# Kernel tuning notes

Hardware: AMD Instinct MI355X
Metric: run time of the kernel (lower is better)

Reference implementation:

```python
import jax, jax.numpy as jnp
import numpy as np

N_NODES = 50000
N_EDGES = 400000
F_IN = 70
E_DIM = 4
HID = 128
HEADS = 4


def _add_self_loops(src, dst, edge_attr, n):
    # PyG GATConv(add_self_loops=True, fill_value='mean' when edge_dim is set):
    # self-loop edge_attr = per-dst-node mean of incoming edge_attr.
    cnt = jax.ops.segment_sum(jnp.ones((src.shape[0],), edge_attr.dtype), dst, n)
    loop_attr = jax.ops.segment_sum(edge_attr, dst, n) / jnp.clip(cnt, 1.0)[:, None]
    loop = jnp.arange(n, dtype=src.dtype)
    return (jnp.concatenate([src, loop]), jnp.concatenate([dst, loop]),
            jnp.concatenate([edge_attr, loop_attr], axis=0))


def _gat_layer(x, src, dst, e_attr, W, a_src, a_dst, We, a_edge, b, concat):
    # W: [in, H*D]; a_src/a_dst/a_edge: [H, D]; We: [edge_dim, H*D]
    n = x.shape[0]
    H, D = a_src.shape
    xs = (x @ W).reshape(n, H, D)                      # [N,H,D]
    s_src = jnp.einsum('nhd,hd->nh', xs, a_src)        # [N,H]
    s_dst = jnp.einsum('nhd,hd->nh', xs, a_dst)
    ee = (e_attr @ We).reshape(-1, H, D)               # [E,H,D]
    s_edge = jnp.einsum('ehd,hd->eh', ee, a_edge)
    alpha = jax.nn.leaky_relu(s_src[src] + s_dst[dst] + s_edge, 0.2)  # [E,H]
    # segment softmax over edges grouped by destination node
    m = jax.ops.segment_max(alpha, dst, n)
    m = jnp.where(jnp.isfinite(m), m, 0.0)
    ex = jnp.exp(alpha - m[dst])
    denom = jax.ops.segment_sum(ex, dst, n)
    alpha = ex / (denom[dst] + 1e-16)
    msg = xs[src] * alpha[..., None]                   # [E,H,D] -- dominant traffic
    agg = jax.ops.segment_sum(msg, dst, n)             # [N,H,D]
    out = agg.reshape(n, H * D) if concat else agg.mean(axis=1)
    return out + b


def _layer_norm(x, g, b, eps=1e-5):
    mu = x.mean(-1, keepdims=True)
    var = ((x - mu) ** 2).mean(-1, keepdims=True)
    return (x - mu) * jax.lax.rsqrt(var + eps) * g + b


def setup_inputs() -> dict:
    key = jax.random.key(0)
    ks = jax.random.split(key, 24)
    f32 = jnp.float32
    node_features = jax.random.normal(ks[0], (N_NODES, F_IN), f32)
    edge_index = jax.random.randint(ks[1], (2, N_EDGES), 0, N_NODES, jnp.int32)
    edge_attr = jax.random.uniform(ks[2], (N_EDGES, E_DIM), f32)
    s = 0.1
    return {
        'node_features': node_features,
        'edge_index': edge_index,
        'edge_attr': edge_attr,
        'W1': jax.random.normal(ks[3], (F_IN, HEADS * HID), f32) * s,
        'as1': jax.random.normal(ks[4], (HEADS, HID), f32) * s,
        'ad1': jax.random.normal(ks[5], (HEADS, HID), f32) * s,
        'We1': jax.random.normal(ks[6], (E_DIM, HEADS * HID), f32) * s,
        'ae1': jax.random.normal(ks[7], (HEADS, HID), f32) * s,
        'b1': jnp.zeros((HEADS * HID,), f32),
        # GAT layer 2: 512 -> 128, 1 head, mean
        'W2': jax.random.normal(ks[8], (HEADS * HID, HID), f32) * s,
        'as2': jax.random.normal(ks[9], (1, HID), f32) * s,
        'ad2': jax.random.normal(ks[10], (1, HID), f32) * s,
        'We2': jax.random.normal(ks[11], (E_DIM, HID), f32) * s,
        'ae2': jax.random.normal(ks[12], (1, HID), f32) * s,
        'b2': jnp.zeros((HID,), f32),
        'ln_g': jnp.ones((HID,), f32),
        'ln_b': jnp.zeros((HID,), f32),
        'pw': jax.random.normal(ks[13], (HID, 8), f32) * s,
        'pb': jnp.zeros((8,), f32),
        'dw': jax.random.normal(ks[14], (HID, 4), f32) * s,
        'db': jnp.zeros((4,), f32),
    }


def reference(node_features, edge_index, edge_attr, W1, as1, ad1, We1, ae1, b1,
              W2, as2, ad2, We2, ae2, b2, ln_g, ln_b, pw, pb, dw, db):
    n = node_features.shape[0]
    src, dst, ea = _add_self_loops(edge_index[0], edge_index[1], edge_attr, n)
    x = jax.nn.gelu(_gat_layer(node_features, src, dst, ea, W1, as1, ad1, We1, ae1, b1, True), approximate=False)
    x = jax.nn.gelu(_gat_layer(x, src, dst, ea, W2, as2, ad2, We2, ae2, b2, False), approximate=False)
    x = _layer_norm(x, ln_g, ln_b)
    return (x @ pw + pb, x @ dw + db)
```

## Files before the change

### kernel.cpp

```cpp
#include <hip/hip_runtime.h>
#include <hip/hip_bf16.h>
#include <math.h>

#define NN 50000
#define NE 400000
#define FIN 70
#define EDIM 4
#define HIDD 128
#define NHEAD 4
constexpr int ET = NE + NN;
constexpr int KP1 = 96;
constexpr int NFP = 72;
constexpr int SCB = (NN + 255) / 256;

constexpr size_t al4(size_t x){ return (x + 3) & ~size_t(3); }
constexpr size_t CNT_O   = 0;
constexpr size_t ZEND    = al4(CNT_O + NN);
constexpr size_t CSR_O   = ZEND;
constexpr size_t BSUM_O  = al4(CSR_O + NN + 1);
constexpr size_t BOFF_O  = al4(BSUM_O + 256);
constexpr size_t EPK_O   = al4(BOFF_O + 256);
constexpr size_t EXF1_O  = al4(EPK_O + (size_t)ET*4);
constexpr size_t EXF2_O  = al4(EXF1_O + (size_t)ET*4);
constexpr size_t SS1_O   = al4(EXF2_O + ET);
constexpr size_t SD1_O   = al4(SS1_O + (size_t)NN*4);
constexpr size_t SS2_O   = al4(SD1_O + (size_t)NN*4);
constexpr size_t SD2_O   = al4(SS2_O + NN);
constexpr size_t CST_O   = al4(SD2_O + NN);
constexpr size_t W1T_O   = al4(CST_O + 2048);
constexpr size_t W2T_O   = al4(W1T_O + 4*128*KP1/2);
constexpr size_t NFB_O   = al4(W2T_O + 128*512/2);
constexpr size_t AGG_O   = al4(NFB_O + (size_t)NN*NFP/2);
constexpr size_t XS2_O   = al4(AGG_O + (size_t)4*NN*KP1/2);

constexpr int VS1 = 0;
constexpr int VD1 = 320;
constexpr int VE1 = 640;
constexpr int VE2 = 656;
constexpr int VS2 = 704;
constexpr int VD2 = 1216;

typedef short s8v __attribute__((ext_vector_type(8)));
typedef float f4v __attribute__((ext_vector_type(4)));

__device__ __forceinline__ unsigned short f2b(float v){
  __hip_bfloat16 b = __float2bfloat16(v);
  return *(unsigned short*)&b;
}
__device__ __forceinline__ float b2f(unsigned u_lo16){
  return __uint_as_float(u_lo16 << 16);
}
__device__ __forceinline__ unsigned pk2(float lo, float hi){
  return (unsigned)f2b(lo) | ((unsigned)f2b(hi) << 16);
}
__device__ __forceinline__ float lrelu(float x){ return x > 0.f ? x : 0.2f * x; }

__device__ __forceinline__ float gelu_fast(float x){
  float z = x * 0.70710678118654752440f;
  float a = fabsf(z);
  float t = 1.f / (1.f + 0.3275911f * a);
  float p = ((((1.061405429f*t - 1.453152027f)*t + 1.421413741f)*t
              - 0.284496736f)*t + 0.254829592f)*t;
  float erfv = 1.f - p * __expf(-a * a);
  erfv = copysignf(erfv, z);
  return 0.5f * x * (1.f + erfv);
}

__global__ void k_deg(const int* __restrict__ ei, int* __restrict__ cnt){
  int e = blockIdx.x * 256 + threadIdx.x;
  if (e >= NE) return;
  atomicAdd(&cnt[ei[NE + e]], 1);
}

__global__ void k_scan1(const int* __restrict__ cnt, int* __restrict__ bsum){
  __shared__ int ws[4];
  int t = threadIdx.x, lane = t & 63, w = t >> 6;
  int i = blockIdx.x * 256 + t;
  int v = (i < NN) ? cnt[i] + 1 : 0;
  for (int o = 32; o; o >>= 1) v += __shfl_down(v, o);
  if (lane == 0) ws[w] = v;
  __syncthreads();
  if (t == 0) bsum[blockIdx.x] = ws[0] + ws[1] + ws[2] + ws[3];
}

__global__ void k_scan2(const int* __restrict__ bsum, int* __restrict__ boff){
  __shared__ int ws[4];
  int t = threadIdx.x, lane = t & 63, w = t >> 6;
  int v = (t < SCB) ? bsum[t] : 0;
  int x = v;
  #pragma unroll
  for (int o = 1; o < 64; o <<= 1){ int u = __shfl_up(x, o); if (lane >= o) x += u; }
  if (lane == 63) ws[w] = x;
  __syncthreads();
  if (w == 0 && lane < 4){
    int y = ws[lane];
    #pragma unroll
    for (int o = 1; o < 4; o <<= 1){ int u = __shfl_up(y, o); if (lane >= o) y += u; }
    ws[lane] = y;
  }
  __syncthreads();
  int incl = x + (w > 0 ? ws[w - 1] : 0);
  if (t < SCB) boff[t] = incl - v;
}

__global__ void k_scan3(const int* __restrict__ cnt, const int* __restrict__ boff,
                        int* __restrict__ csr){
  __shared__ int ws[4];
  int t = threadIdx.x, lane = t & 63, w = t >> 6;
  int i = blockIdx.x * 256 + t;
  int v = (i < NN) ? cnt[i] + 1 : 0;
  int x = v;
  #pragma unroll
  for (int o = 1; o < 64; o <<= 1){ int u = __shfl_up(x, o); if (lane >= o) x += u; }
  if (lane == 63) ws[w] = x;
  __syncthreads();
  if (w == 0 && lane < 4){
    int y = ws[lane];
    #pragma unroll
    for (int o = 1; o < 4; o <<= 1){ int u = __shfl_up(y, o); if (lane >= o) y += u; }
    ws[lane] = y;
  }
  __syncthreads();
  if (i < NN) csr[i + 1] = boff[blockIdx.x] + (w > 0 ? ws[w - 1] : 0) + x;
  if (i == 0) csr[0] = 0;
}

__global__ void k_fill(const int* __restrict__ ei, const float* __restrict__ ea,
                       const int* __restrict__ csr, int* __restrict__ cnt,
                       int4* __restrict__ epk, const float* __restrict__ ss1,
                       const float* __restrict__ sd1, const float* __restrict__ C,
                       float4* __restrict__ exf){
  int e = blockIdx.x * 256 + threadIdx.x;
  if (e >= NE) return;
  int s = ei[e], d = ei[NE + e];
  int r = atomicSub(&cnt[d], 1);
  int p = csr[d] + r - 1;
  float4 a = *(const float4*)&ea[(size_t)e * 4];
  epk[p] = make_int4(s, d, (int)pk2(a.x, a.y), (int)pk2(a.z, a.w));
  float4 ssv = *(const float4*)&ss1[(size_t)s * 4];
  float4 sdv = *(const float4*)&sd1[(size_t)d * 4];
  float e0 = __expf(lrelu(ssv.x + sdv.x + a.x*C[VE1+0] + a.y*C[VE1+4] + a.z*C[VE1+8]  + a.w*C[VE1+12]));
  float e1 = __expf(lrelu(ssv.y + sdv.y + a.x*C[VE1+1] + a.y*C[VE1+5] + a.z*C[VE1+9]  + a.w*C[VE1+13]));
  float e2 = __expf(lrelu(ssv.z + sdv.z + a.x*C[VE1+2] + a.y*C[VE1+6] + a.z*C[VE1+10] + a.w*C[VE1+14]));
  float e3 = __expf(lrelu(ssv.w + sdv.w + a.x*C[VE1+3] + a.y*C[VE1+7] + a.z*C[VE1+11] + a.w*C[VE1+15]));
  exf[p] = make_float4(e0, e1, e2, e3);
}

__global__ void k_loopself(const int* __restrict__ csr, int4* __restrict__ epk,
                           const float* __restrict__ ss1, const float* __restrict__ sd1,
                           const float* __restrict__ C, float4* __restrict__ exf){
  int n = blockIdx.x * 256 + threadIdx.x;
  if (n >= NN) return;
  int a = csr[n], b = csr[n + 1];
  int deg = b - a - 1;
  float s0 = 0.f, s1 = 0.f, s2 = 0.f, s3 = 0.f;
  for (int p = a; p < b - 1; ++p){
    int4 v = epk[p];
    s0 += b2f((unsigned)v.z & 0xffffu); s1 += b2f((unsigned)v.z >> 16);
    s2 += b2f((unsigned)v.w & 0xffffu); s3 += b2f((unsigned)v.w >> 16);
  }
  float inv = 1.f / (float)(deg > 1 ? deg : 1);
  float m0 = s0*inv, m1 = s1*inv, m2 = s2*inv, m3 = s3*inv;
  epk[b - 1] = make_int4(n, n, (int)pk2(m0, m1), (int)pk2(m2, m3));
  float4 ssv = *(const float4*)&ss1[(size_t)n * 4];
  float4 sdv = *(const float4*)&sd1[(size_t)n * 4];
  float e0 = __expf(lrelu(ssv.x + sdv.x + m0*C[VE1+0] + m1*C[VE1+4] + m2*C[VE1+8]  + m3*C[VE1+12]));
  float e1 = __expf(lrelu(ssv.y + sdv.y + m0*C[VE1+1] + m1*C[VE1+5] + m2*C[VE1+9]  + m3*C[VE1+13]));
  float e2 = __expf(lrelu(ssv.z + sdv.z + m0*C[VE1+2] + m1*C[VE1+6] + m2*C[VE1+10] + m3*C[VE1+14]));
  float e3 = __expf(lrelu(ssv.w + sdv.w + m0*C[VE1+3] + m1*C[VE1+7] + m2*C[VE1+11] + m3*C[VE1+15]));
  exf[b - 1] = make_float4(e0, e1, e2, e3);
}

__global__ void k_prep(const float* __restrict__ W1, const float* __restrict__ as1,
                       const float* __restrict__ ad1, const float* __restrict__ We1,
                       const float* __restrict__ ae1, const float* __restrict__ W2,
                       const float* __restrict__ as2, const float* __restrict__ ad2,
                       const float* __restrict__ We2, const float* __restrict__ ae2,
                       float* __restrict__ C){
  int t = threadIdx.x;
  if (t < 280){
    int k = t >> 2, h = t & 3;
    float s = 0.f, d = 0.f;
    for (int dd = 0; dd < 128; ++dd){
      float w = W1[k*512 + h*128 + dd];
      s += w * as1[h*128 + dd];
      d += w * ad1[h*128 + dd];
    }
    C[VS1 + t] = s; C[VD1 + t] = d;
  }
  if (t < 16){
    int k = t >> 2, h = t & 3;
    float s = 0.f;
    for (int dd = 0; dd < 128; ++dd) s += We1[k*512 + h*128 + dd] * ae1[h*128 + dd];
    C[VE1 + t] = s;
  }
  if (t < 4){
    float s = 0.f;
    for (int dd = 0; dd < 128; ++dd) s += We2[t*128 + dd] * ae2[dd];
    C[VE2 + t] = s;
  }
  {
    float s = 0.f, d = 0.f;
    for (int dd = 0; dd < 128; ++dd){
      float w = W2[t*128 + dd];
      s += w * as2[dd];
      d += w * ad2[dd];
    }
    C[VS2 + t] = s; C[VD2 + t] = d;
  }
}

__global__ void k_tw(const float* __restrict__ W1, const float* __restrict__ W2,
                     unsigned short* __restrict__ W1t, unsigned short* __restrict__ W2t){
  int i = blockIdx.x * 256 + threadIdx.x;
  if (i < 4*128*KP1){
    int k = i % KP1, n = (i / KP1) & 127, h = i / (KP1*128);
    float v = (k < FIN) ? W1[k*512 + h*128 + n] : 0.f;
    W1t[i] = f2b(v);
  } else {
    int j = i - 4*128*KP1;
    if (j < 128*512){
      int k = j & 511, n = j >> 9;
      W2t[j] = f2b(W2[k*128 + n]);
    }
  }
}

__global__ __launch_bounds__(256) void k_cnfs1(const float* __restrict__ nf,
    const float* __restrict__ C, unsigned short* __restrict__ nfb,
    float* __restrict__ ss1, float* __restrict__ sd1){
  int lane = threadIdx.x & 63, w = threadIdx.x >> 6;
  int n = blockIdx.x * 4 + w;
  if (n >= NN) return;
  int c0 = lane * 2;
  bool act = lane < 35;
  float v0 = 0.f, v1 = 0.f;
  if (act){
    v0 = nf[(size_t)n * FIN + c0];
    v1 = nf[(size_t)n * FIN + c0 + 1];
  }
  if (lane < 36) *(unsigned*)&nfb[(size_t)n * NFP + c0] = act ? pk2(v0, v1) : 0u;
  float sh[4] = {0,0,0,0}, dh[4] = {0,0,0,0};
  if (act){
    float4 cs0 = *(const float4*)&C[VS1 + c0*4];
    float4 cs1 = *(const float4*)&C[VS1 + (c0+1)*4];
    float4 cd0 = *(const float4*)&C[VD1 + c0*4];
    float4 cd1 = *(const float4*)&C[VD1 + (c0+1)*4];
    sh[0] = v0*cs0.x + v1*cs1.x; sh[1] = v0*cs0.y + v1*cs1.y;
    sh[2] = v0*cs0.z + v1*cs1.z; sh[3] = v0*cs0.w + v1*cs1.w;
    dh[0] = v0*cd0.x + v1*cd1.x; dh[1] = v0*cd0.y + v1*cd1.y;
    dh[2] = v0*cd0.z + v1*cd1.z; dh[3] = v0*cd0.w + v1*cd1.w;
  }
  #pragma unroll
  for (int o = 32; o; o >>= 1){
    #pragma unroll
    for (int h = 0; h < 4; ++h){
      sh[h] += __shfl_xor(sh[h], o);
      dh[h] += __shfl_xor(dh[h], o);
    }
  }
  if (lane == 0){
    *(float4*)&ss1[(size_t)n*4] = make_float4(sh[0], sh[1], sh[2], sh[3]);
    *(float4*)&sd1[(size_t)n*4] = make_float4(dh[0], dh[1], dh[2], dh[3]);
  }
}

__global__ void k_al2(const int4* __restrict__ epk, const float* __restrict__ ss2,
                      const float* __restrict__ sd2, const float* __restrict__ C,
                      float* __restrict__ ex2){
  int p = blockIdx.x * 256 + threadIdx.x;
  if (p >= ET) return;
  int4 pk = epk[p];
  int s = pk.x, d = pk.y;
  float ax = b2f((unsigned)pk.z & 0xffffu), ay = b2f((unsigned)pk.z >> 16);
  float az = b2f((unsigned)pk.w & 0xffffu), aw = b2f((unsigned)pk.w >> 16);
  ex2[p] = __expf(lrelu(ss2[s] + sd2[d] +
             ax*C[VE2] + ay*C[VE2+1] + az*C[VE2+2] + aw*C[VE2+3]));
}

__global__ __launch_bounds__(256) void k_gemm12(
    const unsigned short* __restrict__ agg, const unsigned short* __restrict__ W1t,
    const unsigned short* __restrict__ W2t, const float* __restrict__ b1,
    const float* __restrict__ Cv, unsigned short* __restrict__ xs2b,
    float* __restrict__ ss2, float* __restrict__ sd2){
  __shared__ unsigned short xt[32 * 520];
  __shared__ unsigned short Bs[128 * 40];
  __shared__ unsigned short As[32 * 40];
  int tid = threadIdx.x, lane = tid & 63, w = tid >> 6;
  int wm = w & 1, wn = w >> 1;
  int m15 = lane & 15, rq = lane >> 4;
  int r0 = blockIdx.x * 32;
  constexpr size_t HS = (size_t)NN * KP1;
  for (int h = 0; h < 4; ++h){
    f4v acc[4] = {};
    const unsigned short* Ah = agg + (size_t)h * HS;
    const unsigned short* Wh = W1t + h * 128 * KP1;
    for (int k0 = 0; k0 < KP1; k0 += 32){
      if (tid < 128){
        int r = tid >> 2, c = tid & 3;
        int gr = r0 + r; if (gr >= NN) gr = NN - 1;
        *(uint4*)&As[r*40 + c*8] = *(const uint4*)&Ah[(size_t)gr*KP1 + k0 + c*8];
      }
      #pragma unroll
      for (int i = 0; i < 2; ++i){
        int idx = tid + i*256;
        int r = idx >> 2, c = idx & 3;
        *(uint4*)&Bs[r*40 + c*8] = *(const uint4*)&Wh[r*KP1 + k0 + c*8];
      }
      __syncthreads();
      s8v af = *(const s8v*)&As[(wm*16 + m15)*40 + rq*8];
      #pragma unroll
      for (int ni = 0; ni < 4; ++ni){
        s8v bf = *(const s8v*)&Bs[(wn*64 + ni*16 + m15)*40 + rq*8];
        acc[ni] = __builtin_amdgcn_mfma_f32_16x16x32_bf16(bf, af, acc[ni], 0, 0, 0);
      }
      __syncthreads();
    }
    int lr = wm*16 + m15;
    #pragma unroll
    for (int ni = 0; ni < 4; ++ni){
      int cb = h*128 + wn*64 + ni*16 + rq*4;
      float4 bv = *(const float4*)&b1[cb];
      float v0 = gelu_fast(acc[ni][0] + bv.x);
      float v1 = gelu_fast(acc[ni][1] + bv.y);
      float v2 = gelu_fast(acc[ni][2] + bv.z);
      float v3 = gelu_fast(acc[ni][3] + bv.w);
      *(uint2*)&xt[lr*520 + cb] = make_uint2(pk2(v0,v1), pk2(v2,v3));
    }
  }
  f4v acc2[4] = {};
  for (int k0 = 0; k0 < 512; k0 += 32){
    #pragma unroll
    for (int i = 0; i < 2; ++i){
      int idx = tid + i*256;
      int r = idx >> 2, c = idx & 3;
      *(uint4*)&Bs[r*40 + c*8] = *(const uint4*)&W2t[r*512 + k0 + c*8];
    }
    __syncthreads();
    s8v af = *(const s8v*)&xt[(wm*16 + m15)*520 + k0 + rq*8];
    #pragma unroll
    for (int ni = 0; ni < 4; ++ni){
      s8v bf = *(const s8v*)&Bs[(wn*64 + ni*16 + m15)*40 + rq*8];
      acc2[ni] = __builtin_amdgcn_mfma_f32_16x16x32_bf16(bf, af, acc2[ni], 0, 0, 0);
    }
    __syncthreads();
  }
  int grow = r0 + wm*16 + m15;
  if (grow < NN){
    #pragma unroll
    for (int ni = 0; ni < 4; ++ni){
      int gc = wn*64 + ni*16 + rq*4;
      *(uint2*)&xs2b[(size_t)grow*128 + gc] =
          make_uint2(pk2(acc2[ni][0], acc2[ni][1]), pk2(acc2[ni][2], acc2[ni][3]));
    }
  }
  int row = tid >> 3, ch = tid & 7;
  float sa = 0.f, sdv = 0.f;
  #pragma unroll
  for (int jj = 0; jj < 8; ++jj){
    int j2 = (jj + ch) & 7;
    int cb = ch*64 + j2*8;
    s8v xv = *(const s8v*)&xt[row*520 + cb];
    #pragma unroll
    for (int t2 = 0; t2 < 8; ++t2){
      float xf = b2f((unsigned short)xv[t2]);
      sa  += xf * Cv[VS2 + cb + t2];
      sdv += xf * Cv[VD2 + cb + t2];
    }
  }
  #pragma unroll
  for (int o = 1; o < 8; o <<= 1){ sa += __shfl_xor(sa, o); sdv += __shfl_xor(sdv, o); }
  if (ch == 0 && r0 + row < NN){ ss2[r0 + row] = sa; sd2[r0 + row] = sdv; }
}

__global__ __launch_bounds__(256) void k_aggnf(const int* __restrict__ csr,
    const int4* __restrict__ epk, const float4* __restrict__ exf,
    const unsigned short* __restrict__ nfb, unsigned short* __restrict__ agg){
  int lane = threadIdx.x & 63, w = threadIdx.x >> 6;
  int n = blockIdx.x * 4 + w;
  if (n >= NN) return;
  int off = __builtin_amdgcn_readfirstlane(csr[n]);
  int end = __builtin_amdgcn_readfirstlane(csr[n + 1]);
  int col = lane * 2;
  bool act = lane < 36;
  float d0=0,d1=0,d2=0,d3=0;
  float a00=0,a01=0,a10=0,a11=0,a20=0,a21=0,a30=0,a31=0;
  int p = off;
  for (; p + 2 <= end; p += 2){
    int s0 = epk[p].x, s1 = epk[p+1].x;
    float4 e0 = exf[p], e1 = exf[p+1];
    unsigned u0 = 0, u1 = 0;
    if (act){
      u0 = *(const unsigned*)&nfb[(size_t)s0 * NFP + col];
      u1 = *(const unsigned*)&nfb[(size_t)s1 * NFP + col];
    }
    d0 += e0.x + e1.x; d1 += e0.y + e1.y; d2 += e0.z + e1.z; d3 += e0.w + e1.w;
    float v00 = b2f(u0 & 0xffffu), v01 = b2f(u0 >> 16);
    float v10 = b2f(u1 & 0xffffu), v11 = b2f(u1 >> 16);
    a00 += e0.x*v00 + e1.x*v10; a01 += e0.x*v01 + e1.x*v11;
    a10 += e0.y*v00 + e1.y*v10; a11 += e0.y*v01 + e1.y*v11;
    a20 += e0.z*v00 + e1.z*v10; a21 += e0.z*v01 + e1.z*v11;
    a30 += e0.w*v00 + e1.w*v10; a31 += e0.w*v01 + e1.w*v11;
  }
  if (p < end){
    int s0 = epk[p].x;
    float4 e0 = exf[p];
    unsigned u0 = 0;
    if (act) u0 = *(const unsigned*)&nfb[(size_t)s0 * NFP + col];
    d0 += e0.x; d1 += e0.y; d2 += e0.z; d3 += e0.w;
    float v00 = b2f(u0 & 0xffffu), v01 = b2f(u0 >> 16);
    a00 += e0.x*v00; a01 += e0.x*v01;
    a10 += e0.y*v00; a11 += e0.y*v01;
    a20 += e0.z*v00; a21 += e0.z*v01;
    a30 += e0.w*v00; a31 += e0.w*v01;
  }
  float i0 = 1.f/(d0+1e-16f), i1 = 1.f/(d1+1e-16f);
  float i2 = 1.f/(d2+1e-16f), i3 = 1.f/(d3+1e-16f);
  constexpr size_t HS = (size_t)NN * KP1;
  size_t base = (size_t)n * KP1 + col;
  if (act){
    *(unsigned*)&agg[base]        = pk2(a00*i0, a01*i0);
    *(unsigned*)&agg[base +   HS] = pk2(a10*i1, a11*i1);
    *(unsigned*)&agg[base + 2*HS] = pk2(a20*i2, a21*i2);
    *(unsigned*)&agg[base + 3*HS] = pk2(a30*i3, a31*i3);
  } else if (lane < 48){
    *(unsigned*)&agg[base]        = 0u;
    *(unsigned*)&agg[base +   HS] = 0u;
    *(unsigned*)&agg[base + 2*HS] = 0u;
    *(unsigned*)&agg[base + 3*HS] = 0u;
  }
}

__global__ __launch_bounds__(256) void k_agg2(
    const int* __restrict__ csr, const int4* __restrict__ epk,
    const float* __restrict__ ex2, const unsigned short* __restrict__ xs2b,
    const float* __restrict__ b2, const float* __restrict__ lng,
    const float* __restrict__ lnb, const float* __restrict__ pw,
    const float* __restrict__ pb, const float* __restrict__ dwm,
    const float* __restrict__ dbv, float* __restrict__ out){
  int lane = threadIdx.x & 63, w = threadIdx.x >> 6;
  int n = blockIdx.x * 4 + w;
  if (n >= NN) return;
  int off = __builtin_amdgcn_readfirstlane(csr[n]);
  int end = __builtin_amdgcn_readfirstlane(csr[n + 1]);
  int c0 = lane * 2;
  float acc0 = 0.f, acc1 = 0.f, den = 0.f;
  int p = off;
  for (; p + 4 <= end; p += 4){
    int s0 = epk[p].x, s1 = epk[p+1].x, s2 = epk[p+2].x, s3 = epk[p+3].x;
    float e0 = ex2[p], e1 = ex2[p+1], e2 = ex2[p+2], e3 = ex2[p+3];
    unsigned u0 = *(const unsigned*)&xs2b[(size_t)s0 * 128 + c0];
    unsigned u1 = *(const unsigned*)&xs2b[(size_t)s1 * 128 + c0];
    unsigned u2 = *(const unsigned*)&xs2b[(size_t)s2 * 128 + c0];
    unsigned u3 = *(const unsigned*)&xs2b[(size_t)s3 * 128 + c0];
    den += (e0 + e1) + (e2 + e3);
    acc0 += e0*b2f(u0 & 0xffffu) + e1*b2f(u1 & 0xffffu)
          + e2*b2f(u2 & 0xffffu) + e3*b2f(u3 & 0xffffu);
    acc1 += e0*b2f(u0 >> 16) + e1*b2f(u1 >> 16)
          + e2*b2f(u2 >> 16) + e3*b2f(u3 >> 16);
  }
  for (; p + 2 <= end; p += 2){
    int s0 = epk[p].x, s1 = epk[p+1].x;
    float e0 = ex2[p], e1 = ex2[p+1];
    unsigned u0 = *(const unsigned*)&xs2b[(size_t)s0 * 128 + c0];
    unsigned u1 = *(const unsigned*)&xs2b[(size_t)s1 * 128 + c0];
    den += e0 + e1;
    acc0 += e0*b2f(u0 & 0xffffu) + e1*b2f(u1 & 0xffffu);
    acc1 += e0*b2f(u0 >> 16) + e1*b2f(u1 >> 16);
  }
  if (p < end){
    int s0 = epk[p].x;
    float e0 = ex2[p];
    unsigned u0 = *(const unsigned*)&xs2b[(size_t)s0 * 128 + c0];
    den += e0;
    acc0 += e0*b2f(u0 & 0xffffu);
    acc1 += e0*b2f(u0 >> 16);
  }
  float invd = 1.f / (den + 1e-16f);
  float g0 = gelu_fast(acc0 * invd + b2[c0]);
  float g1 = gelu_fast(acc1 * invd + b2[c0 + 1]);
  float s = g0 + g1;
  #pragma unroll
  for (int o = 32; o; o >>= 1) s += __shfl_xor(s, o);
  float mu = s * (1.f / 128.f);
  float e0 = g0 - mu, e1 = g1 - mu;
  float q = e0*e0 + e1*e1;
  #pragma unroll
  for (int o = 32; o; o >>= 1) q += __shfl_xor(q, o);
  float rstd = rsqrtf(q * (1.f / 128.f) + 1e-5f);
  float y0 = e0 * rstd * lng[c0] + lnb[c0];
  float y1 = e1 * rstd * lng[c0 + 1] + lnb[c0 + 1];
  float pr[12];
  #pragma unroll
  for (int jj = 0; jj < 8; ++jj) pr[jj] = y0 * pw[c0*8 + jj] + y1 * pw[(c0+1)*8 + jj];
  #pragma unroll
  for (int jj = 0; jj < 4; ++jj) pr[8+jj] = y0 * dwm[c0*4 + jj] + y1 * dwm[(c0+1)*4 + jj];
  #pragma unroll
  for (int o = 32; o; o >>= 1)
    #pragma unroll
    for (int jj = 0; jj < 12; ++jj) pr[jj] += __shfl_xor(pr[jj], o);
  if (lane == 0){
    #pragma unroll
    for (int jj = 0; jj < 8; ++jj) out[(size_t)n*8 + jj] = pr[jj] + pb[jj];
    #pragma unroll
    for (int jj = 0; jj < 4; ++jj) out[(size_t)NN*8 + (size_t)n*4 + jj] = pr[8+jj] + dbv[jj];
  }
}

extern "C" void kernel_launch(void* const* d_in, const int* in_sizes, int n_in,
                              void* d_out, int out_size, void* d_ws, size_t ws_size,
                              hipStream_t stream){
  const float* nf  = (const float*)d_in[0];
  const int*   ei  = (const int*)  d_in[1];
  const float* ea  = (const float*)d_in[2];
  const float* W1  = (const float*)d_in[3];
  const float* as1 = (const float*)d_in[4];
  const float* ad1 = (const float*)d_in[5];
  const float* We1 = (const float*)d_in[6];
  const float* ae1 = (const float*)d_in[7];
  const float* b1  = (const float*)d_in[8];
  const float* W2  = (const float*)d_in[9];
  const float* as2 = (const float*)d_in[10];
  const float* ad2 = (const float*)d_in[11];
  const float* We2 = (const float*)d_in[12];
  const float* ae2 = (const float*)d_in[13];
  const float* b2  = (const float*)d_in[14];
  const float* lng = (const float*)d_in[15];
  const float* lnb = (const float*)d_in[16];
  const float* pw  = (const float*)d_in[17];
  const float* pb  = (const float*)d_in[18];
  const float* dw  = (const float*)d_in[19];
  const float* db  = (const float*)d_in[20];
  float* out = (float*)d_out;

  float* wf = (float*)d_ws;
  int*      cnt  = (int*)     (wf + CNT_O);
  int*      csr  = (int*)     (wf + CSR_O);
  int*      bsum = (int*)     (wf + BSUM_O);
  int*      boff = (int*)     (wf + BOFF_O);
  int4*     epk  = (int4*)    (wf + EPK_O);
  float4*   exf1 = (float4*)  (wf + EXF1_O);
  float*    ex2  =            (wf + EXF2_O);
  float*    ss1  =            (wf + SS1_O);
  float*    sd1  =            (wf + SD1_O);
  float*    ss2  =            (wf + SS2_O);
  float*    sd2  =            (wf + SD2_O);
  float*    Cc   =            (wf + CST_O);
  unsigned short* W1t = (unsigned short*)(wf + W1T_O);
  unsigned short* W2t = (unsigned short*)(wf + W2T_O);
  unsigned short* nfb = (unsigned short*)(wf + NFB_O);
  unsigned short* agg = (unsigned short*)(wf + AGG_O);
  unsigned short* xs2b= (unsigned short*)(wf + XS2_O);

  hipMemsetAsync(cnt, 0, NN * sizeof(int), stream);
  k_prep<<<1, 512, 0, stream>>>(W1, as1, ad1, We1, ae1, W2, as2, ad2, We2, ae2, Cc);
  k_tw<<<(4*128*KP1 + 128*512 + 255) / 256, 256, 0, stream>>>(W1, W2, W1t, W2t);
  k_cnfs1<<<(NN + 3) / 4, 256, 0, stream>>>(nf, Cc, nfb, ss1, sd1);
  k_deg<<<(NE + 255) / 256, 256, 0, stream>>>(ei, cnt);
  k_scan1<<<SCB, 256, 0, stream>>>(cnt, bsum);
  k_scan2<<<1, 256, 0, stream>>>(bsum, boff);
  k_scan3<<<SCB, 256, 0, stream>>>(cnt, boff, csr);
  k_fill<<<(NE + 255) / 256, 256, 0, stream>>>(ei, ea, csr, cnt, epk, ss1, sd1, Cc, exf1);
  k_loopself<<<(NN + 255) / 256, 256, 0, stream>>>(csr, epk, ss1, sd1, Cc, exf1);
  k_aggnf<<<(NN + 3) / 4, 256, 0, stream>>>(csr, epk, exf1, nfb, agg);
  k_gemm12<<<(NN + 31) / 32, 256, 0, stream>>>(agg, W1t, W2t, b1, Cc, xs2b, ss2, sd2);
  k_al2<<<(ET + 255) / 256, 256, 0, stream>>>(epk, ss2, sd2, Cc, ex2);
  k_agg2<<<(NN + 3) / 4, 256, 0, stream>>>(csr, epk, ex2, xs2b,
                                           b2, lng, lnb, pw, pb, dw, db, out);
}
```

Baseline: 372.4 us.

## Load GEMM fragments directly from global memory and fuse attention score dot products

```diff
diff --git a/kernel.cpp b/kernel.cpp
--- a/kernel.cpp
+++ b/kernel.cpp
@@ -284,39 +284,31 @@
     const float* __restrict__ Cv, unsigned short* __restrict__ xs2b,
     float* __restrict__ ss2, float* __restrict__ sd2){
   __shared__ unsigned short xt[32 * 520];
-  __shared__ unsigned short Bs[128 * 40];
-  __shared__ unsigned short As[32 * 40];
+  __shared__ float ssp[32][2], sdp[32][2];
   int tid = threadIdx.x, lane = tid & 63, w = tid >> 6;
   int wm = w & 1, wn = w >> 1;
   int m15 = lane & 15, rq = lane >> 4;
   int r0 = blockIdx.x * 32;
+  int lrow = wm * 16 + m15;
+  int grow = r0 + lrow;
+  int growc = grow < NN ? grow : NN - 1;
   constexpr size_t HS = (size_t)NN * KP1;
+  float s2a = 0.f, s2d = 0.f;
+  #pragma unroll
   for (int h = 0; h < 4; ++h){
+    const unsigned short* Ah = agg + (size_t)h * HS + (size_t)growc * KP1;
+    const unsigned short* Wh = W1t + h * 128 * KP1;
     f4v acc[4] = {};
-    const unsigned short* Ah = agg + (size_t)h * HS;
-    const unsigned short* Wh = W1t + h * 128 * KP1;
-    for (int k0 = 0; k0 < KP1; k0 += 32){
-      if (tid < 128){
-        int r = tid >> 2, c = tid & 3;
-        int gr = r0 + r; if (gr >= NN) gr = NN - 1;
-        *(uint4*)&As[r*40 + c*8] = *(const uint4*)&Ah[(size_t)gr*KP1 + k0 + c*8];
-      }
-      #pragma unroll
-      for (int i = 0; i < 2; ++i){
-        int idx = tid + i*256;
-        int r = idx >> 2, c = idx & 3;
-        *(uint4*)&Bs[r*40 + c*8] = *(const uint4*)&Wh[r*KP1 + k0 + c*8];
-      }
-      __syncthreads();
-      s8v af = *(const s8v*)&As[(wm*16 + m15)*40 + rq*8];
+    #pragma unroll
+    for (int kk = 0; kk < 3; ++kk){
+      int k0 = kk * 32;
+      s8v af = *(const s8v*)&Ah[k0 + rq*8];
       #pragma unroll
       for (int ni = 0; ni < 4; ++ni){
-        s8v bf = *(const s8v*)&Bs[(wn*64 + ni*16 + m15)*40 + rq*8];
+        s8v bf = *(const s8v*)&Wh[(wn*64 + ni*16 + m15)*KP1 + k0 + rq*8];
         acc[ni] = __builtin_amdgcn_mfma_f32_16x16x32_bf16(bf, af, acc[ni], 0, 0, 0);
       }
-      __syncthreads();
-    }
-    int lr = wm*16 + m15;
+    }
     #pragma unroll
     for (int ni = 0; ni < 4; ++ni){
       int cb = h*128 + wn*64 + ni*16 + rq*4;
@@ -325,27 +317,31 @@
       float v1 = gelu_fast(acc[ni][1] + bv.y);
       float v2 = gelu_fast(acc[ni][2] + bv.z);
       float v3 = gelu_fast(acc[ni][3] + bv.w);
-      *(uint2*)&xt[lr*520 + cb] = make_uint2(pk2(v0,v1), pk2(v2,v3));
-    }
+      float4 cs = *(const float4*)&Cv[VS2 + cb];
+      float4 cd = *(const float4*)&Cv[VD2 + cb];
+      s2a += v0*cs.x + v1*cs.y + v2*cs.z + v3*cs.w;
+      s2d += v0*cd.x + v1*cd.y + v2*cd.z + v3*cd.w;
+      *(uint2*)&xt[lrow*520 + cb] = make_uint2(pk2(v0,v1), pk2(v2,v3));
+    }
+  }
+  s2a += __shfl_xor(s2a, 16); s2a += __shfl_xor(s2a, 32);
+  s2d += __shfl_xor(s2d, 16); s2d += __shfl_xor(s2d, 32);
+  if (rq == 0){ ssp[lrow][wn] = s2a; sdp[lrow][wn] = s2d; }
+  __syncthreads();
+  if (tid < 32 && r0 + tid < NN){
+    ss2[r0 + tid] = ssp[tid][0] + ssp[tid][1];
+    sd2[r0 + tid] = sdp[tid][0] + sdp[tid][1];
   }
   f4v acc2[4] = {};
+  #pragma unroll 4
   for (int k0 = 0; k0 < 512; k0 += 32){
-    #pragma unroll
-    for (int i = 0; i < 2; ++i){
-      int idx = tid + i*256;
-      int r = idx >> 2, c = idx & 3;
-      *(uint4*)&Bs[r*40 + c*8] = *(const uint4*)&W2t[r*512 + k0 + c*8];
-    }
-    __syncthreads();
-    s8v af = *(const s8v*)&xt[(wm*16 + m15)*520 + k0 + rq*8];
+    s8v af = *(const s8v*)&xt[lrow*520 + k0 + rq*8];
     #pragma unroll
     for (int ni = 0; ni < 4; ++ni){
-      s8v bf = *(const s8v*)&Bs[(wn*64 + ni*16 + m15)*40 + rq*8];
+      s8v bf = *(const s8v*)&W2t[(wn*64 + ni*16 + m15)*512 + k0 + rq*8];
       acc2[ni] = __builtin_amdgcn_mfma_f32_16x16x32_bf16(bf, af, acc2[ni], 0, 0, 0);
     }
-    __syncthreads();
-  }
-  int grow = r0 + wm*16 + m15;
+  }
   if (grow < NN){
     #pragma unroll
     for (int ni = 0; ni < 4; ++ni){
@@ -354,23 +350,6 @@
           make_uint2(pk2(acc2[ni][0], acc2[ni][1]), pk2(acc2[ni][2], acc2[ni][3]));
     }
   }
-  int row = tid >> 3, ch = tid & 7;
-  float sa = 0.f, sdv = 0.f;
-  #pragma unroll
-  for (int jj = 0; jj < 8; ++jj){
-    int j2 = (jj + ch) & 7;
-    int cb = ch*64 + j2*8;
-    s8v xv = *(const s8v*)&xt[row*520 + cb];
-    #pragma unroll
-    for (int t2 = 0; t2 < 8; ++t2){
-      float xf = b2f((unsigned short)xv[t2]);
-      sa  += xf * Cv[VS2 + cb + t2];
-      sdv += xf * Cv[VD2 + cb + t2];
-    }
-  }
-  #pragma unroll
-  for (int o = 1; o < 8; o <<= 1){ sa += __shfl_xor(sa, o); sdv += __shfl_xor(sdv, o); }
-  if (ch == 0 && r0 + row < NN){ ss2[r0 + row] = sa; sd2[r0 + row] = sdv; }
 }
 
 __global__ __launch_bounds__(256) void k_aggnf(const int* __restrict__ csr,
```

Result: slower. 390.2 us (+4.8%).
